# Optimization experiments

Hardware: AMD Instinct MI355X
Metric: run time of the kernel (lower is better)

The kernel has to match this reference:

```python
import jax, jax.numpy as jnp
import numpy as np


def setup_inputs() -> dict:
    key = jax.random.key(0)
    k1, k2 = jax.random.split(key)
    x = jax.random.normal(k1, (2, 8, 32, 32, 64), dtype=jnp.float32)
    gamma = jax.random.normal(k2, (1,), dtype=jnp.float32)
    return {"x": x, "gamma": gamma}


def reference(x, gamma):
    # x: (B, D, H, W, C) -> flatten spatial dims to N = D*H*W
    B, D, H, W, C = x.shape
    N = D * H * W
    q = x.reshape(B, N, C)                       # proj_query (B, N, C)
    # energy = Q @ Q^T : (B, N, N) self-similarity over spatial positions
    energy = jnp.einsum('bnc,bmc->bnm', q, q)
    attn = jax.nn.softmax(energy, axis=-1)       # softmax over last axis (keras default)
    out = jnp.einsum('bnm,bmc->bnc', attn, q)    # attention @ Q -> (B, N, C)
    out = out.reshape(B, D, H, W, C)
    return gamma * out + x
```

## Files before the change

### kernel.cpp

```cpp
#include <hip/hip_runtime.h>
#include <hip/hip_bf16.h>

typedef __attribute__((ext_vector_type(8))) short bf16x8;
typedef __attribute__((ext_vector_type(16))) float f32x16;
typedef __attribute__((ext_vector_type(4))) int int4v;

#define NB 2
#define NN 8192
#define NC 64
#define LOG2E 1.44269504088896340736f
#define INV_LOG2E 0.69314718055994530942f
#define MAXNORM_BOUND 16.0f
#define KSTRIDE 68
#define SKIP_THRESH -110.0f
#define LSPLITC 3
#define SPLIT (1 << LSPLITC)
#define KT_PER (128 / SPLIT)

union I4 { int4v v; unsigned long long u[2]; };

__device__ __forceinline__ bf16x8 lds_ld16(const __hip_bfloat16* p) {
    union { bf16x8 v; unsigned long long u[2]; } r;
    r.u[0] = *(const unsigned long long*)(p);
    r.u[1] = *(const unsigned long long*)(p + 4);
    return r.v;
}

__global__ __launch_bounds__(256) void prep_kernel(
        const float* __restrict__ x,
        __hip_bfloat16* __restrict__ qb) {
    const int i = blockIdx.x * 256 + threadIdx.x;
    const float* src = x + ((size_t)i << 3);
    float4 f0 = *(const float4*)(src);
    float4 f1 = *(const float4*)(src + 4);
    __align__(16) __hip_bfloat16 h[8];
    h[0] = __float2bfloat16(f0.x); h[1] = __float2bfloat16(f0.y);
    h[2] = __float2bfloat16(f0.z); h[3] = __float2bfloat16(f0.w);
    h[4] = __float2bfloat16(f1.x); h[5] = __float2bfloat16(f1.y);
    h[6] = __float2bfloat16(f1.z); h[7] = __float2bfloat16(f1.w);
    *(int4v*)(qb + ((size_t)i << 3)) = *(const int4v*)h;
}

__global__ __launch_bounds__(512, 4) void attn_kernel(
        const __hip_bfloat16* __restrict__ qb,
        float* __restrict__ opart,
        float* __restrict__ lpart) {
    __shared__ __hip_bfloat16 Ks[512][KSTRIDE];

    const int blk   = blockIdx.x;
    const int chunk = blk & (SPLIT - 1);
    const int qw    = (blk >> LSPLITC) & 31;
    const int b     = blk >> (5 + LSPLITC);
    const int q0    = qw << 8;
    const int tid  = threadIdx.x;
    const int wave = tid >> 6;
    const int lane = tid & 63;
    const int n5   = lane & 31;
    const int h    = lane >> 5;
    const int q0w  = q0 + (wave << 5);

    const __hip_bfloat16* kvptr = qb + ((size_t)b << 19);

    const int srow = tid >> 3;
    const int scb  = (tid & 7) << 3;

    const __hip_bfloat16* qrow = kvptr + (((size_t)(q0w + n5)) << 6);
    bf16x8 Qf[4];
#pragma unroll
    for (int step = 0; step < 4; ++step)
        Qf[step] = *(const bf16x8*)(qrow + (step << 4) + (h << 3));

    float mb2, thr;
    {
        float s = 0.f;
#pragma unroll
        for (int step = 0; step < 4; ++step)
#pragma unroll
            for (int j = 0; j < 8; ++j) {
                float f = __uint_as_float(((unsigned)(unsigned short)Qf[step][j]) << 16);
                s += f * f;
            }
        s += __shfl_xor(s, 32);
        mb2 = sqrtf(s) * (MAXNORM_BOUND * LOG2E);
        thr = (SKIP_THRESH + mb2) * INV_LOG2E;
    }

    f32x16 O0 = (f32x16)(0.f), O1 = (f32x16)(0.f);
    float lp = 0.f;
    bool wkeep = false;

    const int kb0 = (chunk * KT_PER) << 6;

    I4 g[8];
#define LDHALF(BASEK) do {                                                        \
        _Pragma("unroll")                                                         \
        for (int j = 0; j < 8; ++j)                                               \
            g[j].v = *(const int4v*)(kvptr +                                      \
                (((size_t)((BASEK) + srow + (j << 6))) << 6) + scb);              \
    } while (0)
#define WRHALF() do {                                                             \
        _Pragma("unroll")                                                         \
        for (int j = 0; j < 8; ++j) {                                             \
            *(unsigned long long*)(&Ks[srow + (j << 6)][scb])     = g[j].u[0];    \
            *(unsigned long long*)(&Ks[srow + (j << 6)][scb + 4]) = g[j].u[1];    \
        }                                                                         \
    } while (0)

#define COMPUTE(tt) do {                                                          \
        f32x16 ST0 = (f32x16)(0.f), ST1 = (f32x16)(0.f);                          \
        _Pragma("unroll")                                                         \
        for (int step = 0; step < 4; ++step) {                                    \
            bf16x8 a0 = lds_ld16(&Ks[((tt) << 6) + n5][(step << 4) + (h << 3)]);  \
            bf16x8 a1 = lds_ld16(&Ks[((tt) << 6) + 32 + n5][(step << 4) + (h << 3)]); \
            ST0 = __builtin_amdgcn_mfma_f32_32x32x16_bf16(a0, Qf[step], ST0, 0, 0, 0); \
            ST1 = __builtin_amdgcn_mfma_f32_32x32x16_bf16(a1, Qf[step], ST1, 0, 0, 0); \
        }                                                                         \
        float mx[8];                                                              \
        _Pragma("unroll")                                                         \
        for (int r = 0; r < 8; ++r)                                               \
            mx[r] = fmaxf(fmaxf(ST0[r], ST0[r + 8]), fmaxf(ST1[r], ST1[r + 8])); \
        _Pragma("unroll")                                                         \
        for (int d = 4; d; d >>= 1)                                               \
            _Pragma("unroll")                                                     \
            for (int r = 0; r < d; ++r) mx[r] = fmaxf(mx[r], mx[r + d]);          \
        if (__ballot(mx[0] >= thr) != 0ull) {                                     \
            wkeep = true;                                                         \
            bf16x8 bP[4];                                                         \
            _Pragma("unroll")                                                     \
            for (int s = 0; s < 4; ++s) {                                         \
                _Pragma("unroll")                                                 \
                for (int j = 0; j < 8; ++j) {                                     \
                    const float sv = (s < 2) ? ST0[((s & 1) << 3) + j]            \
                                             : ST1[((s & 1) << 3) + j];           \
                    float p = __builtin_amdgcn_exp2f(fmaf(sv, LOG2E, -mb2));      \
                    lp += p;                                                      \
                    bP[s][j] = __builtin_bit_cast(short, __float2bfloat16(p));    \
                }                                                                 \
            }                                                                     \
            \
            _Pragma("unroll")                                                     \
            for (int s = 0; s < 4; ++s) {                                         \
                bf16x8 a0, a1;                                                    \
                _Pragma("unroll")                                                 \
                for (int j = 0; j < 8; ++j) {                                     \
                    const int kap = ((tt) << 6) + (s << 4) + (h << 2)             \
                                    + (j & 3) + ((j >> 2) << 3);                  \
                    a0[j] = __builtin_bit_cast(short, Ks[kap][n5]);               \
                    a1[j] = __builtin_bit_cast(short, Ks[kap][32 + n5]);          \
                }                                                                 \
                O0 = __builtin_amdgcn_mfma_f32_32x32x16_bf16(a0, bP[s], O0, 0, 0, 0); \
                O1 = __builtin_amdgcn_mfma_f32_32x32x16_bf16(a1, bP[s], O1, 0, 0, 0); \
            }                                                                     \
        }                                                                         \
    } while (0)

    LDHALF(kb0);
    WRHALF();
    __syncthreads();

    LDHALF(kb0 + 512);
    __builtin_amdgcn_sched_barrier(0);

    for (int t = 0; t < 8; ++t) COMPUTE(t);

    __syncthreads();
    WRHALF();
    __syncthreads();

    for (int t = 0; t < 8; ++t) COMPUTE(t);

#undef COMPUTE
#undef WRHALF
#undef LDHALF

    float lsum = lp + __shfl_xor(lp, 32);
    if (h == 0)
        lpart[(chunk << 14) + (b << 13) + q0w + n5] = lsum;

    if (wkeep) {
        float* orow = opart + ((size_t)chunk << 20) +
                      (((size_t)((b << 13) + q0w + n5)) << 6);
#pragma unroll
        for (int g4 = 0; g4 < 4; ++g4) {
            float4 f0 = make_float4(O0[(g4 << 2)], O0[(g4 << 2) + 1],
                                    O0[(g4 << 2) + 2], O0[(g4 << 2) + 3]);
            *(float4*)(orow + (g4 << 3) + (h << 2)) = f0;
            float4 f1 = make_float4(O1[(g4 << 2)], O1[(g4 << 2) + 1],
                                    O1[(g4 << 2) + 2], O1[(g4 << 2) + 3]);
            *(float4*)(orow + 32 + (g4 << 3) + (h << 2)) = f1;
        }
    }
}

__global__ __launch_bounds__(256) void finalize_kernel(
        const float* __restrict__ x,
        const float* __restrict__ gamma_p,
        const float* __restrict__ opart,
        const float* __restrict__ lpart,
        float* __restrict__ out) {
    const int i4 = blockIdx.x * 256 + threadIdx.x;
    const size_t e = (size_t)i4 << 2;
    const int rowg = i4 >> 4;

    float l = 0.f;
    float4 o = make_float4(0.f, 0.f, 0.f, 0.f);
#pragma unroll
    for (int c = 0; c < SPLIT; ++c) {
        const float lc = lpart[(c << 14) + rowg];
        l += lc;
        if (lc != 0.f) {
            float4 t = *(const float4*)(opart + ((size_t)c << 20) + e);
            o.x += t.x; o.y += t.y; o.z += t.z; o.w += t.w;
        }
    }
    const float inv = 1.0f / l;
    const float gm = gamma_p[0];
    float4 xin = *(const float4*)(x + e);
    float4 r;
    r.x = gm * (o.x * inv) + xin.x;
    r.y = gm * (o.y * inv) + xin.y;
    r.z = gm * (o.z * inv) + xin.z;
    r.w = gm * (o.w * inv) + xin.w;
    *(float4*)(out + e) = r;
}

extern "C" void kernel_launch(void* const* d_in, const int* in_sizes, int n_in,
                              void* d_out, int out_size, void* d_ws, size_t ws_size,
                              hipStream_t stream) {
    const float* x     = (const float*)d_in[0];
    const float* gamma = (const float*)d_in[1];
    float* out = (float*)d_out;

    __hip_bfloat16* qb = (__hip_bfloat16*)d_ws;
    float* opart = (float*)((char*)d_ws + (size_t)2 * 1024 * 1024);
    float* lpart = opart + ((size_t)SPLIT << 20);

    prep_kernel<<<512, 256, 0, stream>>>(x, qb);
    attn_kernel<<<NB * 32 * SPLIT, 512, 0, stream>>>(qb, opart, lpart);
    finalize_kernel<<<(NB * NN * NC / 4) / 256, 256, 0, stream>>>(x, gamma, opart, lpart, out);
}
```

Baseline: 92.57 us.

## Split slab into score-only scan pass then recompute only kept tiles

Each slab phase now first computes QK^T scores for all 8 tiles in a non-unrolled loop just to build a bitmask of tiles passing the skip threshold, then revisits only the kept tiles, recomputing the scores and doing the exp and PV MFMAs. The global-load prefetch of the second half overlapping compute of the first half is removed; loads now happen after a barrier. The aim is a smaller code body and lower register pressure, which could allow better occupancy. The cost is recomputing the QK MFMAs for kept tiles and losing the load/compute overlap.

```diff
diff --git a/kernel.cpp b/kernel.cpp
--- a/kernel.cpp
+++ b/kernel.cpp
@@ -91,14 +91,12 @@
 
     const int kb0 = (chunk * KT_PER) << 6;
 
-    I4 g[8];
-#define LDHALF(BASEK) do {                                                        \
+#define STAGE(BASEK) do {                                                         \
+        I4 g[8];                                                                  \
         _Pragma("unroll")                                                         \
         for (int j = 0; j < 8; ++j)                                               \
             g[j].v = *(const int4v*)(kvptr +                                      \
                 (((size_t)((BASEK) + srow + (j << 6))) << 6) + scb);              \
-    } while (0)
-#define WRHALF() do {                                                             \
         _Pragma("unroll")                                                         \
         for (int j = 0; j < 8; ++j) {                                             \
             *(unsigned long long*)(&Ks[srow + (j << 6)][scb])     = g[j].u[0];    \
@@ -106,25 +104,41 @@
         }                                                                         \
     } while (0)
 
-#define COMPUTE(tt) do {                                                          \
-        f32x16 ST0 = (f32x16)(0.f), ST1 = (f32x16)(0.f);                          \
-        _Pragma("unroll")                                                         \
-        for (int step = 0; step < 4; ++step) {                                    \
-            bf16x8 a0 = lds_ld16(&Ks[((tt) << 6) + n5][(step << 4) + (h << 3)]);  \
-            bf16x8 a1 = lds_ld16(&Ks[((tt) << 6) + 32 + n5][(step << 4) + (h << 3)]); \
-            ST0 = __builtin_amdgcn_mfma_f32_32x32x16_bf16(a0, Qf[step], ST0, 0, 0, 0); \
-            ST1 = __builtin_amdgcn_mfma_f32_32x32x16_bf16(a1, Qf[step], ST1, 0, 0, 0); \
+#define SLABPHASE() do {                                                          \
+        unsigned km = 0;                                                          \
+        _Pragma("clang loop unroll(disable)")                                     \
+        for (int t = 0; t < 8; ++t) {                                             \
+            f32x16 ST0 = (f32x16)(0.f), ST1 = (f32x16)(0.f);                      \
+            _Pragma("unroll")                                                     \
+            for (int step = 0; step < 4; ++step) {                                \
+                bf16x8 a0 = lds_ld16(&Ks[(t << 6) + n5][(step << 4) + (h << 3)]); \
+                bf16x8 a1 = lds_ld16(&Ks[(t << 6) + 32 + n5][(step << 4) + (h << 3)]); \
+                ST0 = __builtin_amdgcn_mfma_f32_32x32x16_bf16(a0, Qf[step], ST0, 0, 0, 0); \
+                ST1 = __builtin_amdgcn_mfma_f32_32x32x16_bf16(a1, Qf[step], ST1, 0, 0, 0); \
+            }                                                                     \
+            float mx[8];                                                          \
+            _Pragma("unroll")                                                     \
+            for (int r = 0; r < 8; ++r)                                           \
+                mx[r] = fmaxf(fmaxf(ST0[r], ST0[r + 8]),                          \
+                              fmaxf(ST1[r], ST1[r + 8]));                         \
+            _Pragma("unroll")                                                     \
+            for (int d = 4; d; d >>= 1)                                           \
+                _Pragma("unroll")                                                 \
+                for (int r = 0; r < d; ++r) mx[r] = fmaxf(mx[r], mx[r + d]);      \
+            if (__ballot(mx[0] >= thr) != 0ull) km |= (1u << t);                  \
         }                                                                         \
-        float mx[8];                                                              \
-        _Pragma("unroll")                                                         \
-        for (int r = 0; r < 8; ++r)                                               \
-            mx[r] = fmaxf(fmaxf(ST0[r], ST0[r + 8]), fmaxf(ST1[r], ST1[r + 8])); \
-        _Pragma("unroll")                                                         \
-        for (int d = 4; d; d >>= 1)                                               \
-            _Pragma("unroll")                                                     \
-            for (int r = 0; r < d; ++r) mx[r] = fmaxf(mx[r], mx[r + d]);          \
-        if (__ballot(mx[0] >= thr) != 0ull) {                                     \
+        while (km) {                                                              \
+            const int t = __builtin_ctz(km);                                      \
+            km &= km - 1;                                                         \
             wkeep = true;                                                         \
+            f32x16 ST0 = (f32x16)(0.f), ST1 = (f32x16)(0.f);                      \
+            _Pragma("unroll")                                                     \
+            for (int step = 0; step < 4; ++step) {                                \
+                bf16x8 a0 = lds_ld16(&Ks[(t << 6) + n5][(step << 4) + (h << 3)]); \
+                bf16x8 a1 = lds_ld16(&Ks[(t << 6) + 32 + n5][(step << 4) + (h << 3)]); \
+                ST0 = __builtin_amdgcn_mfma_f32_32x32x16_bf16(a0, Qf[step], ST0, 0, 0, 0); \
+                ST1 = __builtin_amdgcn_mfma_f32_32x32x16_bf16(a1, Qf[step], ST1, 0, 0, 0); \
+            }                                                                     \
             bf16x8 bP[4];                                                         \
             _Pragma("unroll")                                                     \
             for (int s = 0; s < 4; ++s) {                                         \
@@ -143,7 +157,7 @@
                 bf16x8 a0, a1;                                                    \
                 _Pragma("unroll")                                                 \
                 for (int j = 0; j < 8; ++j) {                                     \
-                    const int kap = ((tt) << 6) + (s << 4) + (h << 2)             \
+                    const int kap = (t << 6) + (s << 4) + (h << 2)                \
                                     + (j & 3) + ((j >> 2) << 3);                  \
                     a0[j] = __builtin_bit_cast(short, Ks[kap][n5]);               \
                     a1[j] = __builtin_bit_cast(short, Ks[kap][32 + n5]);          \
@@ -154,24 +168,17 @@
         }                                                                         \
     } while (0)
 
-    LDHALF(kb0);
-    WRHALF();
+    STAGE(kb0);
     __syncthreads();
-
-    LDHALF(kb0 + 512);
-    __builtin_amdgcn_sched_barrier(0);
-
-    for (int t = 0; t < 8; ++t) COMPUTE(t);
+    SLABPHASE();
 
     __syncthreads();
-    WRHALF();
+    STAGE(kb0 + 512);
     __syncthreads();
-
-    for (int t = 0; t < 8; ++t) COMPUTE(t);
-
-#undef COMPUTE
-#undef WRHALF
-#undef LDHALF
+    SLABPHASE();
+
+#undef SLABPHASE
+#undef STAGE
 
     float lsum = lp + __shfl_xor(lp, 32);
     if (h == 0)
```

Measured after the change: 93.35 us. Within noise of the previous version (+0.8%).
